# Kernel tuning notes

Measured on AMD Instinct MI355X. Metric: run time of the kernel, lower is better.

## Reference

```python
import jax, jax.numpy as jnp
import numpy as np

CONTEXT = 10  # symmetric_mask default; self.context is NOT used in call()
SCALE = 16.0  # hard-coded divisor in the source
NEG = 1e9


def setup_inputs() -> dict:
    key = jax.random.key(0)
    k1, k2, k3, k4 = jax.random.split(key, 4)
    B, N, D = 2, 4096, 512
    H, dh = 8, 64
    x = jax.random.normal(k1, (B, N, D), dtype=jnp.float32)
    Wq = jax.random.normal(k2, (H, D, dh), dtype=jnp.float32) * 1e-4
    Wv = jax.random.normal(k3, (H, D, dh), dtype=jnp.float32) * 1e-4
    Wup = jax.random.normal(k4, (H * dh, D), dtype=jnp.float32) * 1e-4
    return {"x": x, "Wq": Wq, "Wv": Wv, "Wup": Wup}


def reference(x, Wq, Wv, Wup):
    B, N, D = x.shape
    H, _, dh = Wq.shape
    # Per-head projections (no bias), vectorized over heads
    Q = jnp.einsum('bnd,hdk->bhnk', x, Wq)  # [B,H,N,dh]
    V = jnp.einsum('bnd,hdk->bhnk', x, Wv)  # [B,H,N,dh]
    # Full score matrix Q @ V^T / 16 (V doubles as keys in this module)
    scores = jnp.einsum('bhnk,bhmk->bhnm', Q, V) / SCALE  # [B,H,N,N]
    # Symmetric band mask: |i-j| <= CONTEXT and |i-j| > 0 (diagonal excluded)
    idx = jnp.arange(N)
    diff = jnp.abs(idx[:, None] - idx[None, :])
    mask = (diff <= CONTEXT) & (diff > 0)  # [N,N]
    scores = scores - NEG * (~mask).astype(scores.dtype)
    weights = jax.nn.softmax(scores, axis=-1)
    C = jnp.einsum('bhnm,bhmk->bhnk', weights, V)  # [B,H,N,dh]
    heads = C.transpose(0, 2, 1, 3).reshape(B, N, H * dh)  # concat heads
    return heads @ Wup  # [B,N,D]
```

## Files before the change

### kernel.cpp

```cpp
#include <hip/hip_runtime.h>
#include <math.h>

#define N_TOK 4096
#define DMODEL 512
#define NHEAD 8
#define DHEAD 64
#define CTX 10
#define NROW 8192

typedef __bf16 bf16x4 __attribute__((ext_vector_type(4)));
typedef __bf16 bf16x8 __attribute__((ext_vector_type(8)));
typedef float  f32x4  __attribute__((ext_vector_type(4)));

#define GLOAD_LDS16(g, l) __builtin_amdgcn_global_load_lds(                 \
    (const __attribute__((address_space(1))) void*)(g),                     \
    (__attribute__((address_space(3))) void*)(l), 16, 0, 0)

__global__ __launch_bounds__(256) void conv_w(const float* __restrict__ Wq,
                                              const float* __restrict__ Wv,
                                              const float* __restrict__ Wup,
                                              __bf16* __restrict__ Wtqv,
                                              __bf16* __restrict__ Wtup)
{
    __shared__ float T[64][65];
    const int tid = threadIdx.x;
    const int bid = blockIdx.x;

    const float* src;
    __bf16* dstBase;
    int k0, rowBase, srcStride;
    if (bid < 128) {
        k0 = (bid & 7) * 64;
        const int h   = (bid >> 3) & 7;
        const int mat = bid >> 6;
        src = (mat ? Wv : Wq) + (size_t)h * DMODEL * DHEAD;
        dstBase = Wtqv;
        rowBase = mat * 512 + h * 64;
        srcStride = DHEAD;
    } else {
        const int b2 = bid - 128;
        k0 = (b2 & 7) * 64;
        const int n0 = (b2 >> 3) * 64;
        src = Wup + n0;
        dstBase = Wtup;
        rowBase = n0;
        srcStride = DMODEL;
    }

#pragma unroll
    for (int it = 0; it < 4; it++) {
        const int kr = it * 16 + (tid >> 4);
        const int c4 = (tid & 15) * 4;
        const float4 v = *(const float4*)(src + (size_t)(k0 + kr) * srcStride + c4);
        T[kr][c4 + 0] = v.x; T[kr][c4 + 1] = v.y;
        T[kr][c4 + 2] = v.z; T[kr][c4 + 3] = v.w;
    }
    __syncthreads();
    const int c   = tid >> 2;
    const int kk0 = (tid & 3) * 16;
    __bf16* dst = dstBase + (size_t)(rowBase + c) * DMODEL + k0 + kk0;
    bf16x8 o0, o1;
#pragma unroll
    for (int j = 0; j < 8; j++) o0[j] = (__bf16)T[kk0 + j][c];
#pragma unroll
    for (int j = 0; j < 8; j++) o1[j] = (__bf16)T[kk0 + 8 + j][c];
    *(bf16x8*)dst = o0;
    *(bf16x8*)(dst + 8) = o1;
}

__global__ __launch_bounds__(256) void gemm_qv_mfma(
    const float* __restrict__ x,
    const __bf16* __restrict__ Wt,
    __bf16* __restrict__ Qt,
    __bf16* __restrict__ Vt)
{
    __shared__ __align__(16) __bf16 As[128 * 32];
    __shared__ __align__(16) __bf16 Bs[64 * 32];

    const int tid  = threadIdx.x;
    const int w    = tid >> 6;
    const int lane = tid & 63;
    const int lm   = lane & 15;
    const int q    = lane >> 4;
    const int bid  = blockIdx.x;
    const int row0 = (bid & 63) * 128;
    const int col0 = (bid >> 6) * 64;

    const int asr = tid >> 3;
    const int asc = (tid & 7) * 4;
    const float* gA = x + (size_t)(row0 + asr) * DMODEL + asc;

    const int sr = lane >> 2;
    const int sc = (lane & 3) * 8;
    const __bf16* gB0 = Wt + (size_t)(col0 + w * 16 + sr) * DMODEL + sc;
    __bf16* lB0 = Bs + (w * 16) * 32;

    f32x4 acc[2][4];
#pragma unroll
    for (int i = 0; i < 2; i++)
#pragma unroll
        for (int j = 0; j < 4; j++) acc[i][j] = (f32x4){0.f, 0.f, 0.f, 0.f};

    for (int k0 = 0; k0 < DMODEL; k0 += 32) {
        float4 a[4];
#pragma unroll
        for (int p = 0; p < 4; p++)
            a[p] = *(const float4*)(gA + (size_t)p * 32 * DMODEL);
        gA += 32;

        __syncthreads();
#pragma unroll
        for (int p = 0; p < 4; p++) {
            bf16x4 o;
            o[0] = (__bf16)a[p].x; o[1] = (__bf16)a[p].y;
            o[2] = (__bf16)a[p].z; o[3] = (__bf16)a[p].w;
            *(bf16x4*)&As[(asr + p * 32) * 32 + asc] = o;
        }
        GLOAD_LDS16(gB0, lB0);
        gB0 += 32;
        __syncthreads();

        bf16x8 af[2], bfr[4];
#pragma unroll
        for (int mi = 0; mi < 2; mi++)
            af[mi] = *(const bf16x8*)&As[(w * 32 + mi * 16 + lm) * 32 + q * 8];
#pragma unroll
        for (int ni = 0; ni < 4; ni++)
            bfr[ni] = *(const bf16x8*)&Bs[(ni * 16 + lm) * 32 + q * 8];
#pragma unroll
        for (int mi = 0; mi < 2; mi++)
#pragma unroll
            for (int ni = 0; ni < 4; ni++)
                acc[mi][ni] = __builtin_amdgcn_mfma_f32_16x16x32_bf16(
                    af[mi], bfr[ni], acc[mi][ni], 0, 0, 0);
    }

#pragma unroll
    for (int ni = 0; ni < 4; ni++) {
        const int c  = col0 + ni * 16 + lm;
        const int cc = c & 511;
        __bf16* outB = (c < 512 ? Qt : Vt);
#pragma unroll
        for (int mi = 0; mi < 2; mi++) {
            const int m  = row0 + w * 32 + mi * 16 + q * 4;
            const int bb = m >> 12;
            const int nt = m & (N_TOK - 1);
            bf16x4 o;
            o[0] = (__bf16)acc[mi][ni][0];
            o[1] = (__bf16)acc[mi][ni][1];
            o[2] = (__bf16)acc[mi][ni][2];
            o[3] = (__bf16)acc[mi][ni][3];
            *(bf16x4*)(outB + ((size_t)(bb * 512 + cc)) * N_TOK + nt) = o;
        }
    }
}

#define VSTRIDE 97
__global__ __launch_bounds__(256) void attn_band(
    const __bf16* __restrict__ Qt,
    const __bf16* __restrict__ Vt,
    __bf16* __restrict__ Hb16)
{
    __shared__ float Vs[64 * VSTRIDE];

    const int tid  = threadIdx.x;
    const int bh   = blockIdx.x >> 6;
    const int tile = blockIdx.x & 63;
    const int i0   = tile * 64;
    const int b    = bh >> 3;
    const int h    = bh & 7;

    const __bf16* vband = Vt + (size_t)bh * DHEAD * N_TOK;
    const int tok0 = i0 - 16;
#pragma unroll
    for (int it = 0; it < 3; it++) {
        const int idx = it * 256 + tid;
        const int k   = idx / 12;
        const int s8  = idx - k * 12;
        const int tokg = tok0 + s8 * 8;
        const int tokc = min(max(tokg, 0), N_TOK - 8);
        const bf16x8 v = *(const bf16x8*)(vband + (size_t)k * N_TOK + tokc);
        float* dst = &Vs[k * VSTRIDE + s8 * 8];
#pragma unroll
        for (int e = 0; e < 8; e++) dst[e] = (float)v[e];
    }

    const int lane = tid & 63;
    const int wv   = tid >> 6;
    const int il   = lane & 15;
    const int p    = lane >> 4;
    const int i    = i0 + wv * 16 + il;
    const int slot0 = wv * 16 + il + 6;

    const __bf16* qbase = Qt + ((size_t)bh * DHEAD + p * 16) * N_TOK;
    float qv[16];
#pragma unroll
    for (int k = 0; k < 16; k++) qv[k] = (float)qbase[(size_t)k * N_TOK + i];

    __syncthreads();

    float c[16];
#pragma unroll
    for (int k = 0; k < 16; k++) c[k] = 0.f;
    float Z = 0.f;

#pragma unroll 3
    for (int d = 0; d < 2 * CTX + 1; d++) {
        const float* vrow = &Vs[p * 16 * VSTRIDE + slot0 + d];
        float v[16];
#pragma unroll
        for (int k = 0; k < 16; k++) v[k] = vrow[k * VSTRIDE];
        float s = 0.f;
#pragma unroll
        for (int k = 0; k < 16; k++) s += qv[k] * v[k];
        s += __shfl_xor(s, 16, 64);
        s += __shfl_xor(s, 32, 64);

        const int j = i + d - CTX;
        const bool valid = (d != CTX) && (j >= 0) && (j < N_TOK);
        const float w = valid ? __expf(s * 0.0625f) : 0.f;
        Z += w;
#pragma unroll
        for (int k = 0; k < 16; k++) c[k] += w * v[k];
    }

    const float inv = 1.f / Z;
    __bf16* dst = Hb16 + ((size_t)(b * N_TOK + i)) * DMODEL + h * DHEAD + p * 16;
    bf16x8 o0, o1;
#pragma unroll
    for (int k = 0; k < 8; k++) o0[k] = (__bf16)(c[k] * inv);
#pragma unroll
    for (int k = 0; k < 8; k++) o1[k] = (__bf16)(c[8 + k] * inv);
    *(bf16x8*)dst = o0;
    *(bf16x8*)(dst + 8) = o1;
}

__global__ __launch_bounds__(256) void gemm_out_mfma(
    const __bf16* __restrict__ Hb,
    const __bf16* __restrict__ Wt,
    float* __restrict__ out)
{
    __shared__ __align__(16) __bf16 As[128 * 32];
    __shared__ __align__(16) __bf16 Bs[64 * 32];

    const int tid  = threadIdx.x;
    const int w    = tid >> 6;
    const int lane = tid & 63;
    const int lm   = lane & 15;
    const int q    = lane >> 4;
    const int bid  = blockIdx.x;
    const int row0 = (bid & 63) * 128;
    const int col0 = (bid >> 6) * 64;

    const int sr = lane >> 2;
    const int sc = (lane & 3) * 8;
    const __bf16* gA0 = Hb + (size_t)(row0 + w * 32 +  0 + sr) * DMODEL + sc;
    const __bf16* gA1 = Hb + (size_t)(row0 + w * 32 + 16 + sr) * DMODEL + sc;
    const __bf16* gB0 = Wt + (size_t)(col0 + w * 16 + sr) * DMODEL + sc;
    __bf16* lA0 = As + (w * 32 +  0) * 32;
    __bf16* lA1 = As + (w * 32 + 16) * 32;
    __bf16* lB0 = Bs + (w * 16) * 32;

    f32x4 acc[2][4];
#pragma unroll
    for (int i = 0; i < 2; i++)
#pragma unroll
        for (int j = 0; j < 4; j++) acc[i][j] = (f32x4){0.f, 0.f, 0.f, 0.f};

    for (int k0 = 0; k0 < DMODEL; k0 += 32) {
        __syncthreads();
        GLOAD_LDS16(gA0, lA0); GLOAD_LDS16(gA1, lA1); GLOAD_LDS16(gB0, lB0);
        gA0 += 32; gA1 += 32; gB0 += 32;
        __syncthreads();

        bf16x8 af[2], bfr[4];
#pragma unroll
        for (int mi = 0; mi < 2; mi++)
            af[mi] = *(const bf16x8*)&As[(w * 32 + mi * 16 + lm) * 32 + q * 8];
#pragma unroll
        for (int ni = 0; ni < 4; ni++)
            bfr[ni] = *(const bf16x8*)&Bs[(ni * 16 + lm) * 32 + q * 8];
#pragma unroll
        for (int mi = 0; mi < 2; mi++)
#pragma unroll
            for (int ni = 0; ni < 4; ni++)
                acc[mi][ni] = __builtin_amdgcn_mfma_f32_16x16x32_bf16(
                    af[mi], bfr[ni], acc[mi][ni], 0, 0, 0);
    }

#pragma unroll
    for (int mi = 0; mi < 2; mi++) {
        const int m0 = row0 + w * 32 + mi * 16 + q * 4;
#pragma unroll
        for (int ni = 0; ni < 4; ni++) {
            const int n = col0 + ni * 16 + lm;
#pragma unroll
            for (int r = 0; r < 4; r++)
                out[(size_t)(m0 + r) * DMODEL + n] = acc[mi][ni][r];
        }
    }
}

extern "C" void kernel_launch(void* const* d_in, const int* in_sizes, int n_in,
                              void* d_out, int out_size, void* d_ws, size_t ws_size,
                              hipStream_t stream)
{
    const float* x   = (const float*)d_in[0];
    const float* Wq  = (const float*)d_in[1];
    const float* Wv  = (const float*)d_in[2];
    const float* Wup = (const float*)d_in[3];
    float* out = (float*)d_out;

    const size_t QV = (size_t)2 * NHEAD * N_TOK * DHEAD;
    __bf16* Qt   = (__bf16*)d_ws;
    __bf16* Vt   = Qt + QV;
    __bf16* Hb16 = Vt + QV;
    __bf16* Wtqv = Hb16 + (size_t)NROW * DMODEL;
    __bf16* Wtup = Wtqv + (size_t)1024 * DMODEL;

    dim3 blk(256);
    conv_w       <<<dim3(192),  blk, 0, stream>>>(Wq, Wv, Wup, Wtqv, Wtup);
    gemm_qv_mfma <<<dim3(1024), blk, 0, stream>>>(x, Wtqv, Qt, Vt);
    attn_band    <<<dim3(1024), blk, 0, stream>>>(Qt, Vt, Hb16);
    gemm_out_mfma<<<dim3(512),  blk, 0, stream>>>(Hb16, Wtup, out);
}
```

Before: 118.0 us.

## Stage full-K weight slab in swizzled LDS and read activations directly from global

Both projection GEMMs now load the block's whole 64xK weight slice into LDS once, using an XOR swizzle to avoid bank conflicts, and then run the K loop without per-step barriers. A fragments are read straight from global memory into registers. Block tiles grow to 256 rows with 4x4 MFMA accumulators per wave. The fp32-to-bf16 conversion of x moves into the weight-conversion prologue kernel so the QV GEMM reads bf16 input. This trades 64KB of LDS per block (lower occupancy) and uncached global A reads for fewer syncs and more reuse per block.

```diff
diff --git a/kernel.cpp b/kernel.cpp
--- a/kernel.cpp
+++ b/kernel.cpp
@@ -19,12 +19,31 @@
 __global__ __launch_bounds__(256) void conv_w(const float* __restrict__ Wq,
                                               const float* __restrict__ Wv,
                                               const float* __restrict__ Wup,
+                                              const float* __restrict__ x,
                                               __bf16* __restrict__ Wtqv,
-                                              __bf16* __restrict__ Wtup)
-{
-    __shared__ float T[64][65];
+                                              __bf16* __restrict__ Wtup,
+                                              __bf16* __restrict__ xb)
+{
     const int tid = threadIdx.x;
     const int bid = blockIdx.x;
+
+    if (bid >= 192) {
+        const int b3 = bid - 192;
+        const float* src = x + (size_t)b3 * 16384;
+        __bf16* dst = xb + (size_t)b3 * 16384;
+#pragma unroll
+        for (int it = 0; it < 16; it++) {
+            const int idx = it * 1024 + tid * 4;
+            const float4 v = *(const float4*)(src + idx);
+            bf16x4 o;
+            o[0] = (__bf16)v.x; o[1] = (__bf16)v.y;
+            o[2] = (__bf16)v.z; o[3] = (__bf16)v.w;
+            *(bf16x4*)(dst + idx) = o;
+        }
+        return;
+    }
+
+    __shared__ float T[64][65];
 
     const float* src;
     __bf16* dstBase;
@@ -69,13 +88,12 @@
 }
 
 __global__ __launch_bounds__(256) void gemm_qv_mfma(
-    const float* __restrict__ x,
+    const __bf16* __restrict__ xb,
     const __bf16* __restrict__ Wt,
     __bf16* __restrict__ Qt,
     __bf16* __restrict__ Vt)
 {
-    __shared__ __align__(16) __bf16 As[128 * 32];
-    __shared__ __align__(16) __bf16 Bs[64 * 32];
+    __shared__ __align__(16) __bf16 Bs[64 * DMODEL];
 
     const int tid  = threadIdx.x;
     const int w    = tid >> 6;
@@ -83,52 +101,43 @@
     const int lm   = lane & 15;
     const int q    = lane >> 4;
     const int bid  = blockIdx.x;
-    const int row0 = (bid & 63) * 128;
-    const int col0 = (bid >> 6) * 64;
-
-    const int asr = tid >> 3;
-    const int asc = (tid & 7) * 4;
-    const float* gA = x + (size_t)(row0 + asr) * DMODEL + asc;
-
-    const int sr = lane >> 2;
-    const int sc = (lane & 3) * 8;
-    const __bf16* gB0 = Wt + (size_t)(col0 + w * 16 + sr) * DMODEL + sc;
-    __bf16* lB0 = Bs + (w * 16) * 32;
-
-    f32x4 acc[2][4];
-#pragma unroll
-    for (int i = 0; i < 2; i++)
+    const int row0 = (bid & 31) * 256;
+    const int col0 = (bid >> 5) * 64;
+
+#pragma unroll
+    for (int r = 0; r < 16; r++) {
+        const int c   = r * 4 + w;
+        const int swz = (c & 7) << 4;
+        const __bf16* src = Wt + (size_t)(col0 + c) * DMODEL
+                          + (((lane * 16) ^ swz) >> 1);
+        GLOAD_LDS16(src, Bs + (size_t)c * DMODEL);
+    }
+
+    const __bf16* gA = xb + (size_t)(row0 + w * 64 + lm) * DMODEL + q * 8;
+    const char* BsB  = (const char*)Bs;
+    const int swzr   = (lm & 7) << 4;
+    const int bbase  = lm * 1024;
+
+    f32x4 acc[4][4];
+#pragma unroll
+    for (int i = 0; i < 4; i++)
 #pragma unroll
         for (int j = 0; j < 4; j++) acc[i][j] = (f32x4){0.f, 0.f, 0.f, 0.f};
 
-    for (int k0 = 0; k0 < DMODEL; k0 += 32) {
-        float4 a[4];
-#pragma unroll
-        for (int p = 0; p < 4; p++)
-            a[p] = *(const float4*)(gA + (size_t)p * 32 * DMODEL);
-        gA += 32;
-
-        __syncthreads();
-#pragma unroll
-        for (int p = 0; p < 4; p++) {
-            bf16x4 o;
-            o[0] = (__bf16)a[p].x; o[1] = (__bf16)a[p].y;
-            o[2] = (__bf16)a[p].z; o[3] = (__bf16)a[p].w;
-            *(bf16x4*)&As[(asr + p * 32) * 32 + asc] = o;
-        }
-        GLOAD_LDS16(gB0, lB0);
-        gB0 += 32;
-        __syncthreads();
-
-        bf16x8 af[2], bfr[4];
-#pragma unroll
-        for (int mi = 0; mi < 2; mi++)
-            af[mi] = *(const bf16x8*)&As[(w * 32 + mi * 16 + lm) * 32 + q * 8];
+    __syncthreads();
+
+#pragma unroll 4
+    for (int kk = 0; kk < 16; kk++) {
+        bf16x8 af[4], bfr[4];
+#pragma unroll
+        for (int mi = 0; mi < 4; mi++)
+            af[mi] = *(const bf16x8*)(gA + (size_t)mi * 16 * DMODEL + kk * 32);
+        const int off = (kk * 64 + q * 16) ^ swzr;
 #pragma unroll
         for (int ni = 0; ni < 4; ni++)
-            bfr[ni] = *(const bf16x8*)&Bs[(ni * 16 + lm) * 32 + q * 8];
-#pragma unroll
-        for (int mi = 0; mi < 2; mi++)
+            bfr[ni] = *(const bf16x8*)(BsB + ni * 16 * 1024 + bbase + off);
+#pragma unroll
+        for (int mi = 0; mi < 4; mi++)
 #pragma unroll
             for (int ni = 0; ni < 4; ni++)
                 acc[mi][ni] = __builtin_amdgcn_mfma_f32_16x16x32_bf16(
@@ -141,8 +150,8 @@
         const int cc = c & 511;
         __bf16* outB = (c < 512 ? Qt : Vt);
 #pragma unroll
-        for (int mi = 0; mi < 2; mi++) {
-            const int m  = row0 + w * 32 + mi * 16 + q * 4;
+        for (int mi = 0; mi < 4; mi++) {
+            const int m  = row0 + w * 64 + mi * 16 + q * 4;
             const int bb = m >> 12;
             const int nt = m & (N_TOK - 1);
             bf16x4 o;
@@ -240,8 +249,7 @@
     const __bf16* __restrict__ Wt,
     float* __restrict__ out)
 {
-    __shared__ __align__(16) __bf16 As[128 * 32];
-    __shared__ __align__(16) __bf16 Bs[64 * 32];
+    __shared__ __align__(16) __bf16 Bs[64 * DMODEL];
 
     const int tid  = threadIdx.x;
     const int w    = tid >> 6;
@@ -249,39 +257,43 @@
     const int lm   = lane & 15;
     const int q    = lane >> 4;
     const int bid  = blockIdx.x;
-    const int row0 = (bid & 63) * 128;
-    const int col0 = (bid >> 6) * 64;
-
-    const int sr = lane >> 2;
-    const int sc = (lane & 3) * 8;
-    const __bf16* gA0 = Hb + (size_t)(row0 + w * 32 +  0 + sr) * DMODEL + sc;
-    const __bf16* gA1 = Hb + (size_t)(row0 + w * 32 + 16 + sr) * DMODEL + sc;
-    const __bf16* gB0 = Wt + (size_t)(col0 + w * 16 + sr) * DMODEL + sc;
-    __bf16* lA0 = As + (w * 32 +  0) * 32;
-    __bf16* lA1 = As + (w * 32 + 16) * 32;
-    __bf16* lB0 = Bs + (w * 16) * 32;
-
-    f32x4 acc[2][4];
-#pragma unroll
-    for (int i = 0; i < 2; i++)
+    const int row0 = (bid & 31) * 256;
+    const int col0 = (bid >> 5) * 64;
+
+#pragma unroll
+    for (int r = 0; r < 16; r++) {
+        const int c   = r * 4 + w;
+        const int swz = (c & 7) << 4;
+        const __bf16* src = Wt + (size_t)(col0 + c) * DMODEL
+                          + (((lane * 16) ^ swz) >> 1);
+        GLOAD_LDS16(src, Bs + (size_t)c * DMODEL);
+    }
+
+    const __bf16* gA = Hb + (size_t)(row0 + w * 64 + lm) * DMODEL + q * 8;
+    const char* BsB  = (const char*)Bs;
+    const int swzr   = (lm & 7) << 4;
+    const int bbase  = lm * 1024;
+
+    f32x4 acc[4][4];
+#pragma unroll
+    for (int i = 0; i < 4; i++)
 #pragma unroll
         for (int j = 0; j < 4; j++) acc[i][j] = (f32x4){0.f, 0.f, 0.f, 0.f};
 
-    for (int k0 = 0; k0 < DMODEL; k0 += 32) {
-        __syncthreads();
-        GLOAD_LDS16(gA0, lA0); GLOAD_LDS16(gA1, lA1); GLOAD_LDS16(gB0, lB0);
-        gA0 += 32; gA1 += 32; gB0 += 32;
-        __syncthreads();
-
-        bf16x8 af[2], bfr[4];
-#pragma unroll
-        for (int mi = 0; mi < 2; mi++)
-            af[mi] = *(const bf16x8*)&As[(w * 32 + mi * 16 + lm) * 32 + q * 8];
+    __syncthreads();
+
+#pragma unroll 4
+    for (int kk = 0; kk < 16; kk++) {
+        bf16x8 af[4], bfr[4];
+#pragma unroll
+        for (int mi = 0; mi < 4; mi++)
+            af[mi] = *(const bf16x8*)(gA + (size_t)mi * 16 * DMODEL + kk * 32);
+        const int off = (kk * 64 + q * 16) ^ swzr;
 #pragma unroll
         for (int ni = 0; ni < 4; ni++)
-            bfr[ni] = *(const bf16x8*)&Bs[(ni * 16 + lm) * 32 + q * 8];
-#pragma unroll
-        for (int mi = 0; mi < 2; mi++)
+            bfr[ni] = *(const bf16x8*)(BsB + ni * 16 * 1024 + bbase + off);
+#pragma unroll
+        for (int mi = 0; mi < 4; mi++)
 #pragma unroll
             for (int ni = 0; ni < 4; ni++)
                 acc[mi][ni] = __builtin_amdgcn_mfma_f32_16x16x32_bf16(
@@ -289,8 +301,8 @@
     }
 
 #pragma unroll
-    for (int mi = 0; mi < 2; mi++) {
-        const int m0 = row0 + w * 32 + mi * 16 + q * 4;
+    for (int mi = 0; mi < 4; mi++) {
+        const int m0 = row0 + w * 64 + mi * 16 + q * 4;
 #pragma unroll
         for (int ni = 0; ni < 4; ni++) {
             const int n = col0 + ni * 16 + lm;
@@ -317,10 +329,11 @@
     __bf16* Hb16 = Vt + QV;
     __bf16* Wtqv = Hb16 + (size_t)NROW * DMODEL;
     __bf16* Wtup = Wtqv + (size_t)1024 * DMODEL;
+    __bf16* xb   = Wtup + (size_t)512 * DMODEL;
 
     dim3 blk(256);
-    conv_w       <<<dim3(192),  blk, 0, stream>>>(Wq, Wv, Wup, Wtqv, Wtup);
-    gemm_qv_mfma <<<dim3(1024), blk, 0, stream>>>(x, Wtqv, Qt, Vt);
+    conv_w       <<<dim3(448),  blk, 0, stream>>>(Wq, Wv, Wup, x, Wtqv, Wtup, xb);
+    gemm_qv_mfma <<<dim3(512),  blk, 0, stream>>>(xb, Wtqv, Qt, Vt);
     attn_band    <<<dim3(1024), blk, 0, stream>>>(Qt, Vt, Hb16);
-    gemm_out_mfma<<<dim3(512),  blk, 0, stream>>>(Hb16, Wtup, out);
-}
+    gemm_out_mfma<<<dim3(256),  blk, 0, stream>>>(Hb16, Wtup, out);
+}
```

After: 128.6 us. 9.0% more time.

## Pre-convert x to bf16, widen GEMM K-tiles to 64 with XOR-swizzled LDS

Applied to the files above, without the earlier changes.

Adds blocks to the weight-conversion kernel that convert x to bf16 in workspace, so the QV GEMM can load A directly into LDS with global_load_lds instead of converting fp32 in registers. Both MFMA GEMMs now use a K-tile of 64 (half the loop iterations and barriers) with an XOR swizzle on LDS columns to avoid bank conflicts on fragment reads. This costs an extra pass over x (fp32 read plus bf16 write) and doubles LDS per block, which may lower occupancy.

```diff
diff --git a/kernel.cpp b/kernel.cpp
--- a/kernel.cpp
+++ b/kernel.cpp
@@ -19,12 +19,31 @@
 __global__ __launch_bounds__(256) void conv_w(const float* __restrict__ Wq,
                                               const float* __restrict__ Wv,
                                               const float* __restrict__ Wup,
+                                              const float* __restrict__ x,
                                               __bf16* __restrict__ Wtqv,
-                                              __bf16* __restrict__ Wtup)
-{
-    __shared__ float T[64][65];
+                                              __bf16* __restrict__ Wtup,
+                                              __bf16* __restrict__ xb)
+{
     const int tid = threadIdx.x;
     const int bid = blockIdx.x;
+
+    if (bid >= 192) {
+        const int b3 = bid - 192;
+        const float* src = x + (size_t)b3 * 16384;
+        __bf16* dst = xb + (size_t)b3 * 16384;
+#pragma unroll
+        for (int it = 0; it < 16; it++) {
+            const int idx = it * 1024 + tid * 4;
+            const float4 v = *(const float4*)(src + idx);
+            bf16x4 o;
+            o[0] = (__bf16)v.x; o[1] = (__bf16)v.y;
+            o[2] = (__bf16)v.z; o[3] = (__bf16)v.w;
+            *(bf16x4*)(dst + idx) = o;
+        }
+        return;
+    }
+
+    __shared__ float T[64][65];
 
     const float* src;
     __bf16* dstBase;
@@ -69,13 +88,13 @@
 }
 
 __global__ __launch_bounds__(256) void gemm_qv_mfma(
-    const float* __restrict__ x,
+    const __bf16* __restrict__ xb,
     const __bf16* __restrict__ Wt,
     __bf16* __restrict__ Qt,
     __bf16* __restrict__ Vt)
 {
-    __shared__ __align__(16) __bf16 As[128 * 32];
-    __shared__ __align__(16) __bf16 Bs[64 * 32];
+    __shared__ __align__(16) __bf16 As[128 * 64];
+    __shared__ __align__(16) __bf16 Bs[64 * 64];
 
     const int tid  = threadIdx.x;
     const int w    = tid >> 6;
@@ -86,14 +105,14 @@
     const int row0 = (bid & 63) * 128;
     const int col0 = (bid >> 6) * 64;
 
-    const int asr = tid >> 3;
-    const int asc = (tid & 7) * 4;
-    const float* gA = x + (size_t)(row0 + asr) * DMODEL + asc;
-
-    const int sr = lane >> 2;
-    const int sc = (lane & 3) * 8;
-    const __bf16* gB0 = Wt + (size_t)(col0 + w * 16 + sr) * DMODEL + sc;
-    __bf16* lB0 = Bs + (w * 16) * 32;
+    const int sxr = lane >> 3;
+    const int sxc = ((lane & 7) ^ sxr) * 8;
+    const __bf16* gA = xb + (size_t)(row0 + w * 32 + sxr) * DMODEL + sxc;
+    const __bf16* gB = Wt + (size_t)(col0 + w * 16 + sxr) * DMODEL + sxc;
+    __bf16* lA = As + w * 32 * 64;
+    __bf16* lB = Bs + w * 16 * 64;
+
+    const int off0 = ((q ^ (lm & 7)) * 8);
 
     f32x4 acc[2][4];
 #pragma unroll
@@ -101,38 +120,38 @@
 #pragma unroll
         for (int j = 0; j < 4; j++) acc[i][j] = (f32x4){0.f, 0.f, 0.f, 0.f};
 
-    for (int k0 = 0; k0 < DMODEL; k0 += 32) {
-        float4 a[4];
-#pragma unroll
-        for (int p = 0; p < 4; p++)
-            a[p] = *(const float4*)(gA + (size_t)p * 32 * DMODEL);
-        gA += 32;
-
+    for (int k0 = 0; k0 < DMODEL; k0 += 64) {
         __syncthreads();
 #pragma unroll
-        for (int p = 0; p < 4; p++) {
-            bf16x4 o;
-            o[0] = (__bf16)a[p].x; o[1] = (__bf16)a[p].y;
-            o[2] = (__bf16)a[p].z; o[3] = (__bf16)a[p].w;
-            *(bf16x4*)&As[(asr + p * 32) * 32 + asc] = o;
-        }
-        GLOAD_LDS16(gB0, lB0);
-        gB0 += 32;
+        for (int g = 0; g < 4; g++)
+            GLOAD_LDS16(gA + (size_t)g * 8 * DMODEL, lA + g * 512);
+#pragma unroll
+        for (int g = 0; g < 2; g++)
+            GLOAD_LDS16(gB + (size_t)g * 8 * DMODEL, lB + g * 512);
+        gA += 64; gB += 64;
         __syncthreads();
 
-        bf16x8 af[2], bfr[4];
-#pragma unroll
-        for (int mi = 0; mi < 2; mi++)
-            af[mi] = *(const bf16x8*)&As[(w * 32 + mi * 16 + lm) * 32 + q * 8];
-#pragma unroll
-        for (int ni = 0; ni < 4; ni++)
-            bfr[ni] = *(const bf16x8*)&Bs[(ni * 16 + lm) * 32 + q * 8];
-#pragma unroll
-        for (int mi = 0; mi < 2; mi++)
-#pragma unroll
-            for (int ni = 0; ni < 4; ni++)
-                acc[mi][ni] = __builtin_amdgcn_mfma_f32_16x16x32_bf16(
-                    af[mi], bfr[ni], acc[mi][ni], 0, 0, 0);
+        bf16x8 af[2][2], bfr[4][2];
+#pragma unroll
+        for (int mi = 0; mi < 2; mi++) {
+            const int r = (w * 32 + mi * 16 + lm) * 64;
+            af[mi][0] = *(const bf16x8*)&As[r + off0];
+            af[mi][1] = *(const bf16x8*)&As[r + (off0 ^ 32)];
+        }
+#pragma unroll
+        for (int ni = 0; ni < 4; ni++) {
+            const int r = (ni * 16 + lm) * 64;
+            bfr[ni][0] = *(const bf16x8*)&Bs[r + off0];
+            bfr[ni][1] = *(const bf16x8*)&Bs[r + (off0 ^ 32)];
+        }
+#pragma unroll
+        for (int kk2 = 0; kk2 < 2; kk2++)
+#pragma unroll
+            for (int mi = 0; mi < 2; mi++)
+#pragma unroll
+                for (int ni = 0; ni < 4; ni++)
+                    acc[mi][ni] = __builtin_amdgcn_mfma_f32_16x16x32_bf16(
+                        af[mi][kk2], bfr[ni][kk2], acc[mi][ni], 0, 0, 0);
     }
 
 #pragma unroll
@@ -240,8 +259,8 @@
     const __bf16* __restrict__ Wt,
     float* __restrict__ out)
 {
-    __shared__ __align__(16) __bf16 As[128 * 32];
-    __shared__ __align__(16) __bf16 Bs[64 * 32];
+    __shared__ __align__(16) __bf16 As[128 * 64];
+    __shared__ __align__(16) __bf16 Bs[64 * 64];
 
     const int tid  = threadIdx.x;
     const int w    = tid >> 6;
@@ -252,14 +271,14 @@
     const int row0 = (bid & 63) * 128;
     const int col0 = (bid >> 6) * 64;
 
-    const int sr = lane >> 2;
-    const int sc = (lane & 3) * 8;
-    const __bf16* gA0 = Hb + (size_t)(row0 + w * 32 +  0 + sr) * DMODEL + sc;
-    const __bf16* gA1 = Hb + (size_t)(row0 + w * 32 + 16 + sr) * DMODEL + sc;
-    const __bf16* gB0 = Wt + (size_t)(col0 + w * 16 + sr) * DMODEL + sc;
-    __bf16* lA0 = As + (w * 32 +  0) * 32;
-    __bf16* lA1 = As + (w * 32 + 16) * 32;
-    __bf16* lB0 = Bs + (w * 16) * 32;
+    const int sxr = lane >> 3;
+    const int sxc = ((lane & 7) ^ sxr) * 8;
+    const __bf16* gA = Hb + (size_t)(row0 + w * 32 + sxr) * DMODEL + sxc;
+    const __bf16* gB = Wt + (size_t)(col0 + w * 16 + sxr) * DMODEL + sxc;
+    __bf16* lA = As + w * 32 * 64;
+    __bf16* lB = Bs + w * 16 * 64;
+
+    const int off0 = ((q ^ (lm & 7)) * 8);
 
     f32x4 acc[2][4];
 #pragma unroll
@@ -267,25 +286,38 @@
 #pragma unroll
         for (int j = 0; j < 4; j++) acc[i][j] = (f32x4){0.f, 0.f, 0.f, 0.f};
 
-    for (int k0 = 0; k0 < DMODEL; k0 += 32) {
+    for (int k0 = 0; k0 < DMODEL; k0 += 64) {
         __syncthreads();
-        GLOAD_LDS16(gA0, lA0); GLOAD_LDS16(gA1, lA1); GLOAD_LDS16(gB0, lB0);
-        gA0 += 32; gA1 += 32; gB0 += 32;
+#pragma unroll
+        for (int g = 0; g < 4; g++)
+            GLOAD_LDS16(gA + (size_t)g * 8 * DMODEL, lA + g * 512);
+#pragma unroll
+        for (int g = 0; g < 2; g++)
+            GLOAD_LDS16(gB + (size_t)g * 8 * DMODEL, lB + g * 512);
+        gA += 64; gB += 64;
         __syncthreads();
 
-        bf16x8 af[2], bfr[4];
-#pragma unroll
-        for (int mi = 0; mi < 2; mi++)
-            af[mi] = *(const bf16x8*)&As[(w * 32 + mi * 16 + lm) * 32 + q * 8];
-#pragma unroll
-        for (int ni = 0; ni < 4; ni++)
-            bfr[ni] = *(const bf16x8*)&Bs[(ni * 16 + lm) * 32 + q * 8];
-#pragma unroll
-        for (int mi = 0; mi < 2; mi++)
-#pragma unroll
-            for (int ni = 0; ni < 4; ni++)
-                acc[mi][ni] = __builtin_amdgcn_mfma_f32_16x16x32_bf16(
-                    af[mi], bfr[ni], acc[mi][ni], 0, 0, 0);
+        bf16x8 af[2][2], bfr[4][2];
+#pragma unroll
+        for (int mi = 0; mi < 2; mi++) {
+            const int r = (w * 32 + mi * 16 + lm) * 64;
+            af[mi][0] = *(const bf16x8*)&As[r + off0];
+            af[mi][1] = *(const bf16x8*)&As[r + (off0 ^ 32)];
+        }
+#pragma unroll
+        for (int ni = 0; ni < 4; ni++) {
+            const int r = (ni * 16 + lm) * 64;
+            bfr[ni][0] = *(const bf16x8*)&Bs[r + off0];
+            bfr[ni][1] = *(const bf16x8*)&Bs[r + (off0 ^ 32)];
+        }
+#pragma unroll
+        for (int kk2 = 0; kk2 < 2; kk2++)
+#pragma unroll
+            for (int mi = 0; mi < 2; mi++)
+#pragma unroll
+                for (int ni = 0; ni < 4; ni++)
+                    acc[mi][ni] = __builtin_amdgcn_mfma_f32_16x16x32_bf16(
+                        af[mi][kk2], bfr[ni][kk2], acc[mi][ni], 0, 0, 0);
     }
 
 #pragma unroll
@@ -317,10 +349,11 @@
     __bf16* Hb16 = Vt + QV;
     __bf16* Wtqv = Hb16 + (size_t)NROW * DMODEL;
     __bf16* Wtup = Wtqv + (size_t)1024 * DMODEL;
+    __bf16* xb   = Wtup + (size_t)512 * DMODEL;
 
     dim3 blk(256);
-    conv_w       <<<dim3(192),  blk, 0, stream>>>(Wq, Wv, Wup, Wtqv, Wtup);
-    gemm_qv_mfma <<<dim3(1024), blk, 0, stream>>>(x, Wtqv, Qt, Vt);
+    conv_w       <<<dim3(448),  blk, 0, stream>>>(Wq, Wv, Wup, x, Wtqv, Wtup, xb);
+    gemm_qv_mfma <<<dim3(1024), blk, 0, stream>>>(xb, Wtqv, Qt, Vt);
     attn_band    <<<dim3(1024), blk, 0, stream>>>(Qt, Vt, Hb16);
     gemm_out_mfma<<<dim3(512),  blk, 0, stream>>>(Hb16, Wtup, out);
 }
```

Result: faster. 114.9 us (-2.6%).
